# Kernel optimization log

Hardware: AMD Instinct MI355X
Metric: run time of the kernel (lower is better)

The kernel has to match this reference:

```python
import jax, jax.numpy as jnp
import numpy as np

N = 50000      # nodes
E = 800000     # edges (avg degree 16)
IN = 128       # in_channels
OUT = 64       # out_channels
HID = 2 * OUT  # 128, hidden width of conv1
EPS = 1e-5     # BatchNorm eps


def _edge_norm(edge_index):
    # PyG ChebConv with sym normalization, lambda_max=2: L_hat = -D^{-1/2} A D^{-1/2}
    src, dst = edge_index[0], edge_index[1]
    deg = jax.ops.segment_sum(jnp.ones((E,), jnp.float32), src, num_segments=N)
    dinv = jnp.where(deg > 0, jax.lax.rsqrt(jnp.maximum(deg, 1.0)), 0.0)
    return -dinv[src] * dinv[dst]


def _cheb(x, src, dst, norm, W0, W1, b):
    # K=2 Chebyshev conv: Tx0 = x, Tx1 = L_hat x (sparse propagate)
    tx1 = jax.ops.segment_sum(x[src] * norm[:, None], dst, num_segments=N)
    return x @ W0 + tx1 @ W1 + b


def setup_inputs() -> dict:
    key = jax.random.key(0)
    ks = jax.random.split(key, 14)
    g = lambda k, shp, fan: jax.random.normal(k, shp, jnp.float32) / np.sqrt(fan)
    return {
        "x": jax.random.normal(ks[0], (N, IN), jnp.float32),
        "edge_index": jax.random.randint(ks[1], (2, E), 0, N, dtype=jnp.int32),
        "W1_0": g(ks[2], (IN, HID), IN),
        "W1_1": g(ks[3], (IN, HID), IN),
        "b1": jnp.zeros((HID,), jnp.float32),
        "gamma": jnp.ones((HID,), jnp.float32),
        "beta": jnp.zeros((HID,), jnp.float32),
        "Wmu_0": g(ks[4], (HID, OUT), HID),
        "Wmu_1": g(ks[5], (HID, OUT), HID),
        "b_mu": jnp.zeros((OUT,), jnp.float32),
        "Wls_0": g(ks[6], (HID, OUT), HID),
        "Wls_1": g(ks[7], (HID, OUT), HID),
        "b_ls": jnp.zeros((OUT,), jnp.float32),
    }


def reference(x, edge_index, W1_0, W1_1, b1, gamma, beta,
              Wmu_0, Wmu_1, b_mu, Wls_0, Wls_1, b_ls):
    src, dst = edge_index[0], edge_index[1]
    norm = _edge_norm(edge_index)
    h = _cheb(x, src, dst, norm, W1_0, W1_1, b1)         # [N, HID]
    # BatchNorm1d (training mode: batch statistics over nodes)
    mean = jnp.mean(h, axis=0)
    var = jnp.var(h, axis=0)
    h = (h - mean) * jax.lax.rsqrt(var + EPS) * gamma + beta
    h = jax.nn.relu(h)
    mu = _cheb(h, src, dst, norm, Wmu_0, Wmu_1, b_mu)    # [N, OUT]
    logstd = _cheb(h, src, dst, norm, Wls_0, Wls_1, b_ls)
    return (mu, logstd)
```

## Files before the change

kernel.cpp:

```cpp
#include <hip/hip_runtime.h>
#include <cstddef>
#include <cstdint>

static constexpr int IN_C  = 128;
static constexpr float BN_EPS = 1e-5f;
static constexpr int OUT_C = 64;

static constexpr int CS_C = 32;
static constexpr int CS_R = 8;
static constexpr int CS_RANGE = 6250;
static constexpr int NMAX = 50000;
static constexpr int NHALF = NMAX / 2;

using bf16x8 = __attribute__((ext_vector_type(8))) short;
using f32x4  = __attribute__((ext_vector_type(4))) float;

__device__ __forceinline__ ushort f2bf(float f) {
    uint u = __float_as_uint(f);
    u += 0x7fffu + ((u >> 16) & 1u);
    return (ushort)(u >> 16);
}
__device__ __forceinline__ uint pack2(float a, float b) {
    return (uint)f2bf(a) | ((uint)f2bf(b) << 16);
}
__device__ __forceinline__ float bf_lo(uint v) { return __uint_as_float(v << 16); }
__device__ __forceinline__ float bf_hi(uint v) { return __uint_as_float(v & 0xffff0000u); }

__device__ __forceinline__ int swz8(int row, int g) { return (g ^ ((row >> 1) & 3)) * 8; }

__global__ __launch_bounds__(1024) void hist_conv_k(
    const int* __restrict__ src, const int* __restrict__ dst,
    ushort* __restrict__ hsrc_part, ushort* __restrict__ hdst_part,
    int N, int E, int chunk, int nb_x,
    const float* __restrict__ x, ushort* __restrict__ xb,
    const float* __restrict__ W1_0, const float* __restrict__ W1_1,
    const float* __restrict__ b1,
    const float* __restrict__ Wmu_0, const float* __restrict__ Wmu_1,
    const float* __restrict__ b_mu,
    const float* __restrict__ Wls_0, const float* __restrict__ Wls_1,
    const float* __restrict__ b_ls,
    ushort* __restrict__ Wt1, ushort* __restrict__ Wt2,
    float* __restrict__ bias1, float* __restrict__ bias2) {
    __shared__ uint hp[NHALF];
    int bid = blockIdx.x;
    int tid = threadIdx.x;
    if (bid < 2 * CS_C) {
        bool is_dst = (bid >= CS_C);
        int c = is_dst ? bid - CS_C : bid;
        const int* ea = is_dst ? dst : src;
        ushort* outp = is_dst ? hdst_part : hsrc_part;
        for (int j = tid; j < NHALF; j += 1024) hp[j] = 0u;
        __syncthreads();
        int e0 = c * chunk, e1 = min(e0 + chunk, E);
        for (int i = e0 + tid; i < e1; i += 1024) {
            int s = ea[i];
            atomicAdd(&hp[s >> 1], 1u << ((s & 1) * 16));
        }
        __syncthreads();
        uint* op = (uint*)(outp + (size_t)c * N);
        for (int j = tid; j < N / 2; j += 1024) op[j] = hp[j];
    } else if (bid < 2 * CS_C + nb_x) {
        int i = (bid - 2 * CS_C) * 1024 + tid;
        if (i < N * 64) {
            float2 v = ((const float2*)x)[i];
            ((uint*)xb)[i] = pack2(v.x, v.y);
        }
    } else {
        int idx = (bid - 2 * CS_C - nb_x) * 1024 + tid;
        int which = idx >> 15;
        int c = (idx >> 8) & 127;
        int k = idx & 255;
        if (which == 0) {
            float v = (k < 128) ? W1_0[k * 128 + c] : W1_1[(k - 128) * 128 + c];
            Wt1[c * 256 + k] = f2bf(v);
            if (k == 0) bias1[c] = b1[c];
        } else {
            float v;
            if (c < 64) v = (k < 128) ? Wmu_0[k * 64 + c] : Wmu_1[(k - 128) * 64 + c];
            else        v = (k < 128) ? Wls_0[k * 64 + (c - 64)] : Wls_1[(k - 128) * 64 + (c - 64)];
            Wt2[c * 256 + k] = f2bf(v);
            if (k == 0) bias2[c] = (c < 64) ? b_mu[c] : b_ls[c - 64];
        }
    }
}

__global__ __launch_bounds__(256) void count_k(
    const ushort* __restrict__ hsrc_part, const ushort* __restrict__ hdst_part,
    float* __restrict__ dinv, int* __restrict__ cnt_dst,
    int* __restrict__ bsum, float* __restrict__ stats, int N) {
    __shared__ int sw[4];
    int tid = threadIdx.x;
    if (blockIdx.x == 0) stats[tid] = 0.f;
    int v = blockIdx.x * 256 + tid;
    int b = 0;
    if (v < N) {
        int a = 0;
        for (int c = 0; c < CS_C; ++c) {
            a += hsrc_part[(size_t)c * N + v];
            b += hdst_part[(size_t)c * N + v];
        }
        dinv[v] = (a > 0) ? rsqrtf((float)a) : 0.f;
        cnt_dst[v] = b;
    }
    int t = b;
    #pragma unroll
    for (int off = 1; off < 64; off <<= 1) t += __shfl_xor(t, off, 64);
    if ((tid & 63) == 0) sw[tid >> 6] = t;
    __syncthreads();
    if (tid == 0) bsum[blockIdx.x] = sw[0] + sw[1] + sw[2] + sw[3];
}

__global__ __launch_bounds__(256) void phase3_k(
    const int* __restrict__ cnt, const int* __restrict__ bsum,
    int* __restrict__ row_ptr, const ushort* __restrict__ hdst_part,
    int* __restrict__ offs, int n, int nb) {
    __shared__ int sbp[4];
    __shared__ int swv[4];
    int tid = threadIdx.x;
    int lane = tid & 63, wave = tid >> 6;
    int bv = (tid < nb && tid < (int)blockIdx.x) ? bsum[tid] : 0;
    int t = bv;
    #pragma unroll
    for (int off = 1; off < 64; off <<= 1) t += __shfl_xor(t, off, 64);
    if (lane == 0) sbp[wave] = t;
    int v = blockIdx.x * 256 + tid;
    int c = (v < n) ? cnt[v] : 0;
    int s = c;
    #pragma unroll
    for (int off = 1; off < 64; off <<= 1) {
        int u = __shfl_up(s, off, 64);
        if (lane >= off) s += u;
    }
    if (lane == 63) swv[wave] = s;
    __syncthreads();
    int bpre = sbp[0] + sbp[1] + sbp[2] + sbp[3];
    int wexcl = 0;
    for (int w = 0; w < wave; ++w) wexcl += swv[w];
    int st = bpre + wexcl + (s - c);
    if (v < n) row_ptr[v + 1] = st + c;
    if (v == 0) row_ptr[0] = 0;
    int r = st;
    for (int ch = 0; ch < CS_C; ++ch) {
        size_t idx = (size_t)ch * n + v;
        if (v < n) {
            offs[idx] = r;
            r += hdst_part[idx];
        }
    }
}

__global__ __launch_bounds__(1024) void scatter_k(
    const int* __restrict__ src, const int* __restrict__ dst,
    const int* __restrict__ off, ushort* __restrict__ col,
    int N, int E, int chunk, int range) {
    __shared__ int cur[CS_RANGE];
    int c = blockIdx.x & (CS_C - 1);
    int r = blockIdx.x / CS_C;
    int base = r * range;
    int hi = min(base + range, N);
    int rsz = hi - base;
    for (int j = threadIdx.x; j < rsz; j += 1024)
        cur[j] = off[(size_t)c * N + base + j];
    __syncthreads();
    int e0 = c * chunk, e1 = min(e0 + chunk, E);
    for (int i = e0 + threadIdx.x; i < e1; i += 1024) {
        int t = dst[i];
        if (t >= base && t < hi) {
            int pos = atomicAdd(&cur[t - base], 1);
            col[pos] = (ushort)src[i];
        }
    }
}

#define FMA8(V, D)                                                            \
  { float v0_ = bf_lo((V).x), v1_ = bf_hi((V).x), v2_ = bf_lo((V).y),         \
          v3_ = bf_hi((V).y), v4_ = bf_lo((V).z), v5_ = bf_hi((V).z),         \
          v6_ = bf_lo((V).w), v7_ = bf_hi((V).w);                             \
    if (MODE == 1) {                                                          \
      v0_ = fmaxf(v0_ * sc[0] + sh[0], 0.f);                                  \
      v1_ = fmaxf(v1_ * sc[1] + sh[1], 0.f);                                  \
      v2_ = fmaxf(v2_ * sc[2] + sh[2], 0.f);                                  \
      v3_ = fmaxf(v3_ * sc[3] + sh[3], 0.f);                                  \
      v4_ = fmaxf(v4_ * sc[4] + sh[4], 0.f);                                  \
      v5_ = fmaxf(v5_ * sc[5] + sh[5], 0.f);                                  \
      v6_ = fmaxf(v6_ * sc[6] + sh[6], 0.f);                                  \
      v7_ = fmaxf(v7_ * sc[7] + sh[7], 0.f);                                  \
    }                                                                         \
    acc[0] += v0_ * (D); acc[1] += v1_ * (D); acc[2] += v2_ * (D);            \
    acc[3] += v3_ * (D); acc[4] += v4_ * (D); acc[5] += v5_ * (D);            \
    acc[6] += v6_ * (D); acc[7] += v7_ * (D); }

template <int MODE>
__global__ __launch_bounds__(256) void fused_pg_k(
    const uint4* __restrict__ xsg,
    const ushort* __restrict__ A0,
    const int* __restrict__ row_ptr, const ushort* __restrict__ colu,
    const float* __restrict__ dinv,
    const ushort* __restrict__ Wt, const float* __restrict__ bias,
    ushort* __restrict__ Cb, float* __restrict__ Cmu, float* __restrict__ Cls,
    float* __restrict__ stats, int n,
    const float* __restrict__ gamma, const float* __restrict__ beta,
    float inv_n) {
    __shared__ ushort sA[64][32];
    __shared__ ushort sW[128][32];
    __shared__ ushort xpL[64][136];
    __shared__ float smS[4][128];
    __shared__ float smQ[4][128];
    __shared__ float sp[256];

    int tid = threadIdx.x;
    int block_row = blockIdx.x * 64;
    int wave = tid >> 6, lane = tid & 63;

    if (MODE == 1) {
        if (tid < 128) {
            float mean = stats[tid] * inv_n;
            float var = stats[128 + tid] * inv_n - mean * mean;
            float s = gamma[tid] * rsqrtf(var + BN_EPS);
            sp[tid] = s;
            sp[128 + tid] = beta[tid] - mean * s;
        }
        __syncthreads();
    }

    {
        int g = lane >> 4, li = lane & 15;
        float sc[8], sh[8];
        if (MODE == 1) {
            #pragma unroll
            for (int j = 0; j < 8; ++j) {
                sc[j] = sp[li * 8 + j];
                sh[j] = sp[128 + li * 8 + j];
            }
        }
        for (int t = 0; t < 16; ++t) {
            int ndl = wave * 16 + t;
            int nd = block_row + ndl;
            float acc[8];
            #pragma unroll
            for (int k = 0; k < 8; ++k) acc[k] = 0.f;
            float scl = 0.f;
            if (nd < n) {
                scl = -dinv[nd];
                int s = row_ptr[nd], e = row_ptr[nd + 1];
                int i = s + g;
                for (; i + 12 < e; i += 16) {
                    int c0 = (int)colu[i];
                    int c1 = (int)colu[i + 4];
                    int c2 = (int)colu[i + 8];
                    int c3 = (int)colu[i + 12];
                    float d0 = dinv[c0], d1 = dinv[c1];
                    float d2 = dinv[c2], d3 = dinv[c3];
                    uint4 v0 = xsg[(size_t)c0 * 16 + li];
                    uint4 v1 = xsg[(size_t)c1 * 16 + li];
                    uint4 v2 = xsg[(size_t)c2 * 16 + li];
                    uint4 v3 = xsg[(size_t)c3 * 16 + li];
                    FMA8(v0, d0); FMA8(v1, d1); FMA8(v2, d2); FMA8(v3, d3);
                }
                for (; i < e; i += 4) {
                    int c0 = (int)colu[i];
                    float d0 = dinv[c0];
                    uint4 v0 = xsg[(size_t)c0 * 16 + li];
                    FMA8(v0, d0);
                }
            }
            #pragma unroll
            for (int k = 0; k < 8; ++k) {
                acc[k] += __shfl_xor(acc[k], 16, 64);
                acc[k] += __shfl_xor(acc[k], 32, 64);
            }
            if (g == 0) {
                uint4 o;
                o.x = pack2(acc[0] * scl, acc[1] * scl);
                o.y = pack2(acc[2] * scl, acc[3] * scl);
                o.z = pack2(acc[4] * scl, acc[5] * scl);
                o.w = pack2(acc[6] * scl, acc[7] * scl);
                *(uint4*)&xpL[ndl][li * 8] = o;
            }
        }
    }
    __syncthreads();

    int col_base = lane & 15;
    int quad = lane >> 4;
    int m_local = wave * 16 + col_base;

    f32x4 acc[8];
    #pragma unroll
    for (int t = 0; t < 8; ++t) acc[t] = (f32x4){0.f, 0.f, 0.f, 0.f};

    for (int k0 = 0; k0 < 256; k0 += 32) {
        {
            int row = tid >> 2, g = tid & 3;
            int grow = block_row + row;
            int kc = k0 + g * 8;
            uint4 v = make_uint4(0, 0, 0, 0);
            if (kc < 128) {
                if (grow < n) {
                    v = *(const uint4*)(A0 + (size_t)grow * 128 + kc);
                    if (MODE == 1) {
                        float a0 = fmaxf(bf_lo(v.x) * sp[kc + 0] + sp[128 + kc + 0], 0.f);
                        float a1 = fmaxf(bf_hi(v.x) * sp[kc + 1] + sp[128 + kc + 1], 0.f);
                        float a2 = fmaxf(bf_lo(v.y) * sp[kc + 2] + sp[128 + kc + 2], 0.f);
                        float a3 = fmaxf(bf_hi(v.y) * sp[kc + 3] + sp[128 + kc + 3], 0.f);
                        float a4 = fmaxf(bf_lo(v.z) * sp[kc + 4] + sp[128 + kc + 4], 0.f);
                        float a5 = fmaxf(bf_hi(v.z) * sp[kc + 5] + sp[128 + kc + 5], 0.f);
                        float a6 = fmaxf(bf_lo(v.w) * sp[kc + 6] + sp[128 + kc + 6], 0.f);
                        float a7 = fmaxf(bf_hi(v.w) * sp[kc + 7] + sp[128 + kc + 7], 0.f);
                        v.x = pack2(a0, a1); v.y = pack2(a2, a3);
                        v.z = pack2(a4, a5); v.w = pack2(a6, a7);
                    }
                }
            } else {
                v = *(const uint4*)&xpL[row][kc - 128];
            }
            *(uint4*)&sA[row][swz8(row, g)] = v;
        }
        #pragma unroll
        for (int i = tid; i < 512; i += 256) {
            int c = i >> 2, g = i & 3;
            *(uint4*)&sW[c][swz8(c, g)] = *(const uint4*)(Wt + (size_t)c * 256 + k0 + g * 8);
        }
        __syncthreads();
        bf16x8 af = *(const bf16x8*)&sA[m_local][swz8(m_local, quad)];
        #pragma unroll
        for (int t = 0; t < 8; ++t) {
            int wr = t * 16 + col_base;
            bf16x8 bfr = *(const bf16x8*)&sW[wr][swz8(wr, quad)];
            acc[t] = __builtin_amdgcn_mfma_f32_16x16x32_bf16(af, bfr, acc[t], 0, 0, 0);
        }
        __syncthreads();
    }

    int row_l = wave * 16 + quad * 4;
    #pragma unroll
    for (int t = 0; t < 8; ++t) {
        int col = t * 16 + col_base;
        float b = bias[col];
        float s = 0.f, q = 0.f;
        #pragma unroll
        for (int r = 0; r < 4; ++r) {
            int grow = block_row + row_l + r;
            if (grow < n) {
                float v = acc[t][r] + b;
                if (MODE == 0) {
                    Cb[(size_t)grow * 128 + col] = f2bf(v);
                    s += v; q += v * v;
                } else {
                    if (col < 64) Cmu[(size_t)grow * 64 + col] = v;
                    else          Cls[(size_t)grow * 64 + (col - 64)] = v;
                }
            }
        }
        if (MODE == 0) {
            s += __shfl_xor(s, 16, 64); s += __shfl_xor(s, 32, 64);
            q += __shfl_xor(q, 16, 64); q += __shfl_xor(q, 32, 64);
            if (quad == 0) { smS[wave][col] = s; smQ[wave][col] = q; }
        }
    }
    if (MODE == 0) {
        __syncthreads();
        if (tid < 128) {
            float s = smS[0][tid] + smS[1][tid] + smS[2][tid] + smS[3][tid];
            float q = smQ[0][tid] + smQ[1][tid] + smQ[2][tid] + smQ[3][tid];
            atomicAdd(&stats[tid], s);
            atomicAdd(&stats[128 + tid], q);
        }
    }
}

extern "C" void kernel_launch(void* const* d_in, const int* in_sizes, int n_in,
                              void* d_out, int out_size, void* d_ws, size_t ws_size,
                              hipStream_t stream) {
    const float* x = (const float*)d_in[0];
    const int* edge_index = (const int*)d_in[1];
    const float* W1_0 = (const float*)d_in[2];
    const float* W1_1 = (const float*)d_in[3];
    const float* b1 = (const float*)d_in[4];
    const float* gamma = (const float*)d_in[5];
    const float* beta = (const float*)d_in[6];
    const float* Wmu_0 = (const float*)d_in[7];
    const float* Wmu_1 = (const float*)d_in[8];
    const float* b_mu = (const float*)d_in[9];
    const float* Wls_0 = (const float*)d_in[10];
    const float* Wls_1 = (const float*)d_in[11];
    const float* b_ls = (const float*)d_in[12];

    const int N = in_sizes[0] / IN_C;
    const int E = in_sizes[1] / 2;
    const int* src = edge_index;
    const int* dst = edge_index + E;

    char* w = (char*)d_ws;
    auto alloc = [&](size_t bytes) {
        char* p = w;
        w += (bytes + 15) & ~(size_t)15;
        return p;
    };
    float* stats = (float*)alloc(256 * 4);
    int* row_ptr = (int*)alloc((size_t)(N + 1) * 4);
    int* bsum    = (int*)alloc(256 * 4);
    float* dinv  = (float*)alloc((size_t)N * 4);
    int* cnt_dst = (int*)alloc((size_t)N * 4);
    ushort* col  = (ushort*)alloc((size_t)E * 2);
    ushort* hsrc_part = (ushort*)alloc((size_t)CS_C * N * 2);
    ushort* hdst_part = (ushort*)alloc((size_t)CS_C * N * 2);
    int* offs    = (int*)alloc((size_t)CS_C * N * 4);
    ushort* x_bf  = (ushort*)alloc((size_t)N * 128 * 2);
    ushort* h_bf  = (ushort*)alloc((size_t)N * 128 * 2);
    ushort* Wt1   = (ushort*)alloc(128 * 256 * 2);
    ushort* Wt2   = (ushort*)alloc(128 * 256 * 2);
    float* bias1  = (float*)alloc(128 * 4);
    float* bias2  = (float*)alloc(128 * 4);

    float* out_mu = (float*)d_out;
    float* out_ls = out_mu + (size_t)N * OUT_C;

    int chunk = (E + CS_C - 1) / CS_C;
    int range = (N + CS_R - 1) / CS_R;
    int NBLK = (N + 255) / 256;
    int nb_x = (N * 64 + 1023) / 1024;
    int nb_w = 64;
    float inv_n = 1.f / (float)N;

    hist_conv_k<<<2 * CS_C + nb_x + nb_w, 1024, 0, stream>>>(
        src, dst, hsrc_part, hdst_part, N, E, chunk, nb_x,
        x, x_bf, W1_0, W1_1, b1, Wmu_0, Wmu_1, b_mu, Wls_0, Wls_1, b_ls,
        Wt1, Wt2, bias1, bias2);
    count_k<<<NBLK, 256, 0, stream>>>(hsrc_part, hdst_part, dinv, cnt_dst, bsum, stats, N);
    phase3_k<<<NBLK, 256, 0, stream>>>(cnt_dst, bsum, row_ptr, hdst_part, offs, N, NBLK);
    scatter_k<<<CS_R * CS_C, 1024, 0, stream>>>(src, dst, offs, col, N, E, chunk, range);

    int gb = (N + 63) / 64;
    fused_pg_k<0><<<gb, 256, 0, stream>>>(
        (const uint4*)x_bf, x_bf, row_ptr, col, dinv, Wt1, bias1,
        h_bf, nullptr, nullptr, stats, N, nullptr, nullptr, 0.f);

    fused_pg_k<1><<<gb, 256, 0, stream>>>(
        (const uint4*)h_bf, h_bf, row_ptr, col, dinv, Wt2, bias2,
        nullptr, out_mu, out_ls, stats, N, gamma, beta, inv_n);
}
```

Before: 278.9 us.

## Replace partitioned LDS histograms with global atomic degree counts and scatter

Removes the per-chunk shared-memory histograms, partial-count arrays and per-chunk offset tables used to build the CSR. Degrees are now counted with global atomics into zeroed arrays, and a single cursor per node drives the scatter through global atomics. This cuts the partial-sum traffic and the redundant range-filtered passes over the edges, at the cost of contended global atomics and a non-deterministic neighbor order within each row.

```diff
diff --git a/kernel.cpp b/kernel.cpp
--- a/kernel.cpp
+++ b/kernel.cpp
@@ -5,12 +5,6 @@
 static constexpr int IN_C  = 128;
 static constexpr float BN_EPS = 1e-5f;
 static constexpr int OUT_C = 64;
-
-static constexpr int CS_C = 32;
-static constexpr int CS_R = 8;
-static constexpr int CS_RANGE = 6250;
-static constexpr int NMAX = 50000;
-static constexpr int NHALF = NMAX / 2;
 
 using bf16x8 = __attribute__((ext_vector_type(8))) short;
 using f32x4  = __attribute__((ext_vector_type(4))) float;
@@ -30,8 +24,8 @@
 
 __global__ __launch_bounds__(1024) void hist_conv_k(
     const int* __restrict__ src, const int* __restrict__ dst,
-    ushort* __restrict__ hsrc_part, ushort* __restrict__ hdst_part,
-    int N, int E, int chunk, int nb_x,
+    int* __restrict__ degs, int* __restrict__ degd,
+    int N, int E, int nb_e, int nb_x,
     const float* __restrict__ x, ushort* __restrict__ xb,
     const float* __restrict__ W1_0, const float* __restrict__ W1_1,
     const float* __restrict__ b1,
@@ -41,32 +35,22 @@
     const float* __restrict__ b_ls,
     ushort* __restrict__ Wt1, ushort* __restrict__ Wt2,
     float* __restrict__ bias1, float* __restrict__ bias2) {
-    __shared__ uint hp[NHALF];
     int bid = blockIdx.x;
     int tid = threadIdx.x;
-    if (bid < 2 * CS_C) {
-        bool is_dst = (bid >= CS_C);
-        int c = is_dst ? bid - CS_C : bid;
-        const int* ea = is_dst ? dst : src;
-        ushort* outp = is_dst ? hdst_part : hsrc_part;
-        for (int j = tid; j < NHALF; j += 1024) hp[j] = 0u;
-        __syncthreads();
-        int e0 = c * chunk, e1 = min(e0 + chunk, E);
+    if (bid < nb_e) {
+        int e0 = bid * 4096, e1 = min(e0 + 4096, E);
         for (int i = e0 + tid; i < e1; i += 1024) {
-            int s = ea[i];
-            atomicAdd(&hp[s >> 1], 1u << ((s & 1) * 16));
-        }
-        __syncthreads();
-        uint* op = (uint*)(outp + (size_t)c * N);
-        for (int j = tid; j < N / 2; j += 1024) op[j] = hp[j];
-    } else if (bid < 2 * CS_C + nb_x) {
-        int i = (bid - 2 * CS_C) * 1024 + tid;
+            atomicAdd(&degs[src[i]], 1);
+            atomicAdd(&degd[dst[i]], 1);
+        }
+    } else if (bid < nb_e + nb_x) {
+        int i = (bid - nb_e) * 1024 + tid;
         if (i < N * 64) {
             float2 v = ((const float2*)x)[i];
             ((uint*)xb)[i] = pack2(v.x, v.y);
         }
     } else {
-        int idx = (bid - 2 * CS_C - nb_x) * 1024 + tid;
+        int idx = (bid - nb_e - nb_x) * 1024 + tid;
         int which = idx >> 15;
         int c = (idx >> 8) & 127;
         int k = idx & 255;
@@ -85,22 +69,18 @@
 }
 
 __global__ __launch_bounds__(256) void count_k(
-    const ushort* __restrict__ hsrc_part, const ushort* __restrict__ hdst_part,
-    float* __restrict__ dinv, int* __restrict__ cnt_dst,
-    int* __restrict__ bsum, float* __restrict__ stats, int N) {
+    const int* __restrict__ degs, const int* __restrict__ degd,
+    float* __restrict__ dinv, int* __restrict__ bsum,
+    float* __restrict__ stats, int N) {
     __shared__ int sw[4];
     int tid = threadIdx.x;
     if (blockIdx.x == 0) stats[tid] = 0.f;
     int v = blockIdx.x * 256 + tid;
     int b = 0;
     if (v < N) {
-        int a = 0;
-        for (int c = 0; c < CS_C; ++c) {
-            a += hsrc_part[(size_t)c * N + v];
-            b += hdst_part[(size_t)c * N + v];
-        }
+        int a = degs[v];
         dinv[v] = (a > 0) ? rsqrtf((float)a) : 0.f;
-        cnt_dst[v] = b;
+        b = degd[v];
     }
     int t = b;
     #pragma unroll
@@ -112,8 +92,7 @@
 
 __global__ __launch_bounds__(256) void phase3_k(
     const int* __restrict__ cnt, const int* __restrict__ bsum,
-    int* __restrict__ row_ptr, const ushort* __restrict__ hdst_part,
-    int* __restrict__ offs, int n, int nb) {
+    int* __restrict__ row_ptr, int* __restrict__ cursor, int n, int nb) {
     __shared__ int sbp[4];
     __shared__ int swv[4];
     int tid = threadIdx.x;
@@ -137,38 +116,21 @@
     int wexcl = 0;
     for (int w = 0; w < wave; ++w) wexcl += swv[w];
     int st = bpre + wexcl + (s - c);
-    if (v < n) row_ptr[v + 1] = st + c;
+    if (v < n) {
+        row_ptr[v + 1] = st + c;
+        cursor[v] = st;
+    }
     if (v == 0) row_ptr[0] = 0;
-    int r = st;
-    for (int ch = 0; ch < CS_C; ++ch) {
-        size_t idx = (size_t)ch * n + v;
-        if (v < n) {
-            offs[idx] = r;
-            r += hdst_part[idx];
-        }
-    }
 }
 
 __global__ __launch_bounds__(1024) void scatter_k(
     const int* __restrict__ src, const int* __restrict__ dst,
-    const int* __restrict__ off, ushort* __restrict__ col,
-    int N, int E, int chunk, int range) {
-    __shared__ int cur[CS_RANGE];
-    int c = blockIdx.x & (CS_C - 1);
-    int r = blockIdx.x / CS_C;
-    int base = r * range;
-    int hi = min(base + range, N);
-    int rsz = hi - base;
-    for (int j = threadIdx.x; j < rsz; j += 1024)
-        cur[j] = off[(size_t)c * N + base + j];
-    __syncthreads();
-    int e0 = c * chunk, e1 = min(e0 + chunk, E);
+    int* __restrict__ cursor, ushort* __restrict__ col, int E) {
+    int e0 = blockIdx.x * 4096, e1 = min(e0 + 4096, E);
     for (int i = e0 + threadIdx.x; i < e1; i += 1024) {
         int t = dst[i];
-        if (t >= base && t < hi) {
-            int pos = atomicAdd(&cur[t - base], 1);
-            col[pos] = (ushort)src[i];
-        }
+        int pos = atomicAdd(&cursor[t], 1);
+        col[pos] = (ushort)src[i];
     }
 }
 
@@ -398,38 +360,38 @@
         return p;
     };
     float* stats = (float*)alloc(256 * 4);
+    int* degs    = (int*)alloc((size_t)2 * N * 4);
+    int* degd    = degs + N;
     int* row_ptr = (int*)alloc((size_t)(N + 1) * 4);
+    int* cursor  = (int*)alloc((size_t)N * 4);
     int* bsum    = (int*)alloc(256 * 4);
     float* dinv  = (float*)alloc((size_t)N * 4);
-    int* cnt_dst = (int*)alloc((size_t)N * 4);
     ushort* col  = (ushort*)alloc((size_t)E * 2);
-    ushort* hsrc_part = (ushort*)alloc((size_t)CS_C * N * 2);
-    ushort* hdst_part = (ushort*)alloc((size_t)CS_C * N * 2);
-    int* offs    = (int*)alloc((size_t)CS_C * N * 4);
-    ushort* x_bf  = (ushort*)alloc((size_t)N * 128 * 2);
-    ushort* h_bf  = (ushort*)alloc((size_t)N * 128 * 2);
-    ushort* Wt1   = (ushort*)alloc(128 * 256 * 2);
-    ushort* Wt2   = (ushort*)alloc(128 * 256 * 2);
-    float* bias1  = (float*)alloc(128 * 4);
-    float* bias2  = (float*)alloc(128 * 4);
+    ushort* x_bf = (ushort*)alloc((size_t)N * 128 * 2);
+    ushort* h_bf = (ushort*)alloc((size_t)N * 128 * 2);
+    ushort* Wt1  = (ushort*)alloc(128 * 256 * 2);
+    ushort* Wt2  = (ushort*)alloc(128 * 256 * 2);
+    float* bias1 = (float*)alloc(128 * 4);
+    float* bias2 = (float*)alloc(128 * 4);
 
     float* out_mu = (float*)d_out;
     float* out_ls = out_mu + (size_t)N * OUT_C;
 
-    int chunk = (E + CS_C - 1) / CS_C;
-    int range = (N + CS_R - 1) / CS_R;
     int NBLK = (N + 255) / 256;
+    int nb_e = (E + 4095) / 4096;
     int nb_x = (N * 64 + 1023) / 1024;
     int nb_w = 64;
     float inv_n = 1.f / (float)N;
 
-    hist_conv_k<<<2 * CS_C + nb_x + nb_w, 1024, 0, stream>>>(
-        src, dst, hsrc_part, hdst_part, N, E, chunk, nb_x,
+    hipMemsetAsync(degs, 0, (size_t)2 * N * 4, stream);
+
+    hist_conv_k<<<nb_e + nb_x + nb_w, 1024, 0, stream>>>(
+        src, dst, degs, degd, N, E, nb_e, nb_x,
         x, x_bf, W1_0, W1_1, b1, Wmu_0, Wmu_1, b_mu, Wls_0, Wls_1, b_ls,
         Wt1, Wt2, bias1, bias2);
-    count_k<<<NBLK, 256, 0, stream>>>(hsrc_part, hdst_part, dinv, cnt_dst, bsum, stats, N);
-    phase3_k<<<NBLK, 256, 0, stream>>>(cnt_dst, bsum, row_ptr, hdst_part, offs, N, NBLK);
-    scatter_k<<<CS_R * CS_C, 1024, 0, stream>>>(src, dst, offs, col, N, E, chunk, range);
+    count_k<<<NBLK, 256, 0, stream>>>(degs, degd, dinv, bsum, stats, N);
+    phase3_k<<<NBLK, 256, 0, stream>>>(degd, bsum, row_ptr, cursor, N, NBLK);
+    scatter_k<<<nb_e, 1024, 0, stream>>>(src, dst, cursor, col, E);
 
     int gb = (N + 63) / 64;
     fused_pg_k<0><<<gb, 256, 0, stream>>>(
```

Result: slower. 350.3 us (+25.6%).

## Record per-edge rank in histogram to make CSR scatter atomic-free

Applied to the files above, without the earlier changes.

The dst histogram pass now saves the pre-increment count of each edge as a rank, and also accumulates per-256-node block sums into bsum with global atomics. This removes the separate count kernel and lets the scatter kernel compute each edge's position directly as offs+rank, with no shared-memory atomics and no 8x re-reading of the edge list across ranges. The cost is an extra E-sized rank array to write and read, serial sums in the histogram tail, and a memset launch to zero stats and bsum.

```diff
diff --git a/kernel.cpp b/kernel.cpp
--- a/kernel.cpp
+++ b/kernel.cpp
@@ -7,8 +7,6 @@
 static constexpr int OUT_C = 64;
 
 static constexpr int CS_C = 32;
-static constexpr int CS_R = 8;
-static constexpr int CS_RANGE = 6250;
 static constexpr int NMAX = 50000;
 static constexpr int NHALF = NMAX / 2;
 
@@ -31,6 +29,7 @@
 __global__ __launch_bounds__(1024) void hist_conv_k(
     const int* __restrict__ src, const int* __restrict__ dst,
     ushort* __restrict__ hsrc_part, ushort* __restrict__ hdst_part,
+    ushort* __restrict__ rank, int* __restrict__ bsum,
     int N, int E, int chunk, int nb_x,
     const float* __restrict__ x, ushort* __restrict__ xb,
     const float* __restrict__ W1_0, const float* __restrict__ W1_1,
@@ -52,13 +51,31 @@
         for (int j = tid; j < NHALF; j += 1024) hp[j] = 0u;
         __syncthreads();
         int e0 = c * chunk, e1 = min(e0 + chunk, E);
-        for (int i = e0 + tid; i < e1; i += 1024) {
-            int s = ea[i];
-            atomicAdd(&hp[s >> 1], 1u << ((s & 1) * 16));
+        if (is_dst) {
+            for (int i = e0 + tid; i < e1; i += 1024) {
+                int s = ea[i];
+                uint old = atomicAdd(&hp[s >> 1], 1u << ((s & 1) * 16));
+                rank[i] = (ushort)((old >> ((s & 1) * 16)) & 0xffffu);
+            }
+        } else {
+            for (int i = e0 + tid; i < e1; i += 1024) {
+                int s = ea[i];
+                atomicAdd(&hp[s >> 1], 1u << ((s & 1) * 16));
+            }
         }
         __syncthreads();
         uint* op = (uint*)(outp + (size_t)c * N);
         for (int j = tid; j < N / 2; j += 1024) op[j] = hp[j];
+        if (is_dst) {
+            int ngroups = (N + 255) / 256;
+            for (int gj = tid; gj < ngroups; gj += 1024) {
+                int p0 = gj * 128, p1 = min(p0 + 128, NHALF);
+                uint ssum = 0;
+                for (int k = p0; k < p1; ++k) ssum += hp[k];
+                int cg = (int)(ssum & 0xffffu) + (int)(ssum >> 16);
+                if (cg) atomicAdd(&bsum[gj], cg);
+            }
+        }
     } else if (bid < 2 * CS_C + nb_x) {
         int i = (bid - 2 * CS_C) * 1024 + tid;
         if (i < N * 64) {
@@ -84,36 +101,10 @@
     }
 }
 
-__global__ __launch_bounds__(256) void count_k(
+__global__ __launch_bounds__(256) void phase3_k(
     const ushort* __restrict__ hsrc_part, const ushort* __restrict__ hdst_part,
-    float* __restrict__ dinv, int* __restrict__ cnt_dst,
-    int* __restrict__ bsum, float* __restrict__ stats, int N) {
-    __shared__ int sw[4];
-    int tid = threadIdx.x;
-    if (blockIdx.x == 0) stats[tid] = 0.f;
-    int v = blockIdx.x * 256 + tid;
-    int b = 0;
-    if (v < N) {
-        int a = 0;
-        for (int c = 0; c < CS_C; ++c) {
-            a += hsrc_part[(size_t)c * N + v];
-            b += hdst_part[(size_t)c * N + v];
-        }
-        dinv[v] = (a > 0) ? rsqrtf((float)a) : 0.f;
-        cnt_dst[v] = b;
-    }
-    int t = b;
-    #pragma unroll
-    for (int off = 1; off < 64; off <<= 1) t += __shfl_xor(t, off, 64);
-    if ((tid & 63) == 0) sw[tid >> 6] = t;
-    __syncthreads();
-    if (tid == 0) bsum[blockIdx.x] = sw[0] + sw[1] + sw[2] + sw[3];
-}
-
-__global__ __launch_bounds__(256) void phase3_k(
-    const int* __restrict__ cnt, const int* __restrict__ bsum,
-    int* __restrict__ row_ptr, const ushort* __restrict__ hdst_part,
-    int* __restrict__ offs, int n, int nb) {
+    const int* __restrict__ bsum, float* __restrict__ dinv,
+    int* __restrict__ row_ptr, int* __restrict__ offs, int n, int nb) {
     __shared__ int sbp[4];
     __shared__ int swv[4];
     int tid = threadIdx.x;
@@ -124,7 +115,19 @@
     for (int off = 1; off < 64; off <<= 1) t += __shfl_xor(t, off, 64);
     if (lane == 0) sbp[wave] = t;
     int v = blockIdx.x * 256 + tid;
-    int c = (v < n) ? cnt[v] : 0;
+    int hd[CS_C];
+    int c = 0;
+    if (v < n) {
+        int sdeg = 0;
+        #pragma unroll
+        for (int ch = 0; ch < CS_C; ++ch) {
+            int d = hdst_part[(size_t)ch * n + v];
+            hd[ch] = d;
+            c += d;
+            sdeg += hsrc_part[(size_t)ch * n + v];
+        }
+        dinv[v] = (sdeg > 0) ? rsqrtf((float)sdeg) : 0.f;
+    }
     int s = c;
     #pragma unroll
     for (int off = 1; off < 64; off <<= 1) {
@@ -137,38 +140,28 @@
     int wexcl = 0;
     for (int w = 0; w < wave; ++w) wexcl += swv[w];
     int st = bpre + wexcl + (s - c);
-    if (v < n) row_ptr[v + 1] = st + c;
+    if (v < n) {
+        row_ptr[v + 1] = st + c;
+        int r = st;
+        #pragma unroll
+        for (int ch = 0; ch < CS_C; ++ch) {
+            offs[(size_t)ch * n + v] = r;
+            r += hd[ch];
+        }
+    }
     if (v == 0) row_ptr[0] = 0;
-    int r = st;
-    for (int ch = 0; ch < CS_C; ++ch) {
-        size_t idx = (size_t)ch * n + v;
-        if (v < n) {
-            offs[idx] = r;
-            r += hdst_part[idx];
-        }
-    }
 }
 
 __global__ __launch_bounds__(1024) void scatter_k(
     const int* __restrict__ src, const int* __restrict__ dst,
-    const int* __restrict__ off, ushort* __restrict__ col,
-    int N, int E, int chunk, int range) {
-    __shared__ int cur[CS_RANGE];
-    int c = blockIdx.x & (CS_C - 1);
-    int r = blockIdx.x / CS_C;
-    int base = r * range;
-    int hi = min(base + range, N);
-    int rsz = hi - base;
-    for (int j = threadIdx.x; j < rsz; j += 1024)
-        cur[j] = off[(size_t)c * N + base + j];
-    __syncthreads();
-    int e0 = c * chunk, e1 = min(e0 + chunk, E);
+    const ushort* __restrict__ rank, const int* __restrict__ offs,
+    ushort* __restrict__ col, int E, int chunk, int N) {
+    int e0 = blockIdx.x * 4096, e1 = min(e0 + 4096, E);
     for (int i = e0 + threadIdx.x; i < e1; i += 1024) {
+        int ch = i / chunk;
         int t = dst[i];
-        if (t >= base && t < hi) {
-            int pos = atomicAdd(&cur[t - base], 1);
-            col[pos] = (ushort)src[i];
-        }
+        int pos = offs[(size_t)ch * N + t] + (int)rank[i];
+        col[pos] = (ushort)src[i];
     }
 }
 
@@ -398,11 +391,11 @@
         return p;
     };
     float* stats = (float*)alloc(256 * 4);
+    int* bsum    = (int*)alloc(256 * 4);
     int* row_ptr = (int*)alloc((size_t)(N + 1) * 4);
-    int* bsum    = (int*)alloc(256 * 4);
     float* dinv  = (float*)alloc((size_t)N * 4);
-    int* cnt_dst = (int*)alloc((size_t)N * 4);
     ushort* col  = (ushort*)alloc((size_t)E * 2);
+    ushort* rank = (ushort*)alloc((size_t)E * 2);
     ushort* hsrc_part = (ushort*)alloc((size_t)CS_C * N * 2);
     ushort* hdst_part = (ushort*)alloc((size_t)CS_C * N * 2);
     int* offs    = (int*)alloc((size_t)CS_C * N * 4);
@@ -417,19 +410,21 @@
     float* out_ls = out_mu + (size_t)N * OUT_C;
 
     int chunk = (E + CS_C - 1) / CS_C;
-    int range = (N + CS_R - 1) / CS_R;
     int NBLK = (N + 255) / 256;
+    int nb_e = (E + 4095) / 4096;
     int nb_x = (N * 64 + 1023) / 1024;
     int nb_w = 64;
     float inv_n = 1.f / (float)N;
 
+    hipMemsetAsync(stats, 0, 256 * 4 + 256 * 4, stream);
+
     hist_conv_k<<<2 * CS_C + nb_x + nb_w, 1024, 0, stream>>>(
-        src, dst, hsrc_part, hdst_part, N, E, chunk, nb_x,
+        src, dst, hsrc_part, hdst_part, rank, bsum, N, E, chunk, nb_x,
         x, x_bf, W1_0, W1_1, b1, Wmu_0, Wmu_1, b_mu, Wls_0, Wls_1, b_ls,
         Wt1, Wt2, bias1, bias2);
-    count_k<<<NBLK, 256, 0, stream>>>(hsrc_part, hdst_part, dinv, cnt_dst, bsum, stats, N);
-    phase3_k<<<NBLK, 256, 0, stream>>>(cnt_dst, bsum, row_ptr, hdst_part, offs, N, NBLK);
-    scatter_k<<<CS_R * CS_C, 1024, 0, stream>>>(src, dst, offs, col, N, E, chunk, range);
+    phase3_k<<<NBLK, 256, 0, stream>>>(hsrc_part, hdst_part, bsum,
+                                       dinv, row_ptr, offs, N, NBLK);
+    scatter_k<<<nb_e, 1024, 0, stream>>>(src, dst, rank, offs, col, E, chunk, N);
 
     int gb = (N + 63) / 64;
     fused_pg_k<0><<<gb, 256, 0, stream>>>(
```

Measured after the change: 280.0 us. No clear change (+0.4%).
